# Optimization experiments

Measured on AMD Instinct MI355X. Metric: run time of the kernel, lower is better.

## Reference

```python
import jax, jax.numpy as jnp
import numpy as np
import math

TAU = 1.0          # args.gumbel_tau, used as GMM variance scale in assign()
RD = 64            # args.reduce_dimension
NE = 8             # args.dynamic_nexperts
COMMIT = 0.1       # args.commitment_scale
T, B, C, O = 2048, 8, 512, 512


def setup_inputs() -> dict:
    key = jax.random.key(0)
    ks = jax.random.split(key, 9)
    a = math.sqrt(6.0) / (C + O)  # init for pw_w per dynamic_init_method==1
    return {
        "x": jax.random.normal(ks[0], (T, B, C), jnp.float32),
        "key_feat": jax.random.normal(ks[1], (T, B, C), jnp.float32),  # ignored by forward
        "map_w": jax.random.normal(ks[2], (RD, C), jnp.float32) * math.sqrt(2.0 / (C + RD)),
        "map_b": jnp.zeros((RD,), jnp.float32),
        "centroids": jax.random.normal(ks[3], (NE, RD), jnp.float32) * 0.02,
        "prior": jnp.ones((1, NE), jnp.float32) / NE,
        "pw_w": jax.random.uniform(ks[4], (NE, O * C), jnp.float32, -a, a),
        "bias_w": jax.random.normal(ks[5], (O, C), jnp.float32) * 0.02,
        "bias_b": jnp.zeros((O,), jnp.float32),
    }


def reference(x, key_feat, map_w, map_b, centroids, prior, pw_w, bias_w, bias_b):
    # x: [T, B, C] time-major. key_feat is ignored, matching the original forward.
    Tq, Bq, Cq = x.shape
    N = Tq * Bq
    xf = x.reshape(N, Cq)
    # GMM key projection: [N, RD]
    k = xf @ map_w.T + map_b
    # squared euclid distance to centroids: [N, NE]
    d2 = (jnp.sum(k * k, axis=1, keepdims=True)
          + jnp.sum(centroids * centroids, axis=1)[None, :]
          - 2.0 * (k @ centroids.T))
    # soft GMM responsibilities (training path, no gumbel sampling)
    logresp = (-0.5 * TAU * d2
               - (RD / 2.0) * math.log(2.0 * math.pi * TAU)
               + jnp.log(prior))                                  # [N, NE]
    denom = jax.scipy.special.logsumexp(logresp, axis=-1, keepdims=True)
    resp = jnp.exp(logresp - denom)                               # [N, NE]
    loss = COMMIT * (-jnp.sum(denom))
    # Expert mixture. Original: w = (resp @ pw_w).reshape(T,B,O,C); y = w @ x.
    # Same math, fused order: apply each expert to x, then mix with resp.
    W = pw_w.reshape(NE, O, Cq)
    z = jnp.einsum('ni,eoi->neo', xf, W)        # [N, NE, O] per-expert outputs
    y = jnp.einsum('ne,neo->no', resp, z)       # [N, O]
    y = y.reshape(Tq, Bq, O)
    # dynamic bias: Linear(key_dim -> O) applied to x0
    y = y + x @ bias_w.T + bias_b
    return y, loss
```

## Files before the change

### kernel.cpp

```cpp
#include <hip/hip_runtime.h>
#include <hip/hip_bf16.h>

#define NROWS 16384
#define CC 512
#define OO 512
#define RDIM 64
#define NE 8
#define NEXP 9
#define COMMIT_SCALE 0.1f
#define LOG2PI_TERM 58.81206612509905f

typedef __attribute__((ext_vector_type(8))) short short8;
typedef __attribute__((ext_vector_type(4))) float f32x4;

__device__ __forceinline__ unsigned short f2bf(float f) {
  unsigned int u = __float_as_uint(f);
  u += 0x7fffu + ((u >> 16) & 1u);
  return (unsigned short)(u >> 16);
}
__device__ __forceinline__ unsigned int pkt(float a, float b) {
  return (__float_as_uint(b) & 0xffff0000u) | (__float_as_uint(a) >> 16);
}

__device__ __forceinline__ void gl_lds16(const unsigned short* g, unsigned short* l) {
  __builtin_amdgcn_global_load_lds(
      (const __attribute__((address_space(1))) void*)g,
      (__attribute__((address_space(3))) void*)l, 16, 0, 0);
}

#define P4 524288u
#define B4 65536u
#define NCV ((P4 + B4) / 256u)
#define TB 128u

__global__ __launch_bounds__(256) void k_prep(
    const float* __restrict__ pw, const float* __restrict__ bw,
    const float* __restrict__ mw,
    unsigned short* __restrict__ wb, float* __restrict__ wT4)
{
  unsigned int b = blockIdx.x;
  if (b >= NCV) {
    unsigned int i = (b - NCV) * 256 + threadIdx.x;
    unsigned int j = i >> 9, c = i & 511u;
    wT4[((c >> 2) << 8) + (j << 2) + (c & 3u)] = mw[i];
    return;
  }
  unsigned int i = b * 256 + threadIdx.x;
  const float* src = (i < P4) ? (pw + (size_t)i * 4)
                              : (bw + (size_t)(i - P4) * 4);
  unsigned short* dst = wb + (size_t)i * 4;
  float4 v = *(const float4*)src;
  ushort4 o;
  o.x = f2bf(v.x); o.y = f2bf(v.y); o.z = f2bf(v.z); o.w = f2bf(v.w);
  *(ushort4*)dst = o;
}

__global__ __launch_bounds__(256) void k_assign(
    const float* __restrict__ x,
    const float* __restrict__ wT4,
    const float* __restrict__ map_b,
    const float* __restrict__ cent,
    const float* __restrict__ prior,
    float* __restrict__ resp_out,
    float* __restrict__ loss_acc)
{
  __shared__ float lsum[4];
  const int tid  = threadIdx.x;
  const int wid  = tid >> 6;
  const int lane = tid & 63;
  const int row0 = blockIdx.x * 16 + wid * 4;

  const float* xr0 = x + (size_t)row0 * CC;
  float acc[4] = {0.f, 0.f, 0.f, 0.f};
  #pragma unroll 4
  for (int c0 = 0; c0 < CC; c0 += 4) {
    float4 wv = *(const float4*)&wT4[(c0 << 6) + (lane << 2)];
    #pragma unroll
    for (int r = 0; r < 4; ++r) {
      float4 xv = *(const float4*)(xr0 + r * CC + c0);
      acc[r] += xv.x * wv.x + xv.y * wv.y + xv.z * wv.z + xv.w * wv.w;
    }
  }
  const float mb = map_b[lane];
  float kk[4] = {acc[0] + mb, acc[1] + mb, acc[2] + mb, acc[3] + mb};

  float ce[8], c2[8], lp[8];
  #pragma unroll
  for (int e = 0; e < 8; ++e) {
    ce[e] = cent[e * RDIM + lane];
    float v = ce[e] * ce[e];
    #pragma unroll
    for (int off = 32; off; off >>= 1) v += __shfl_xor(v, off, 64);
    c2[e] = v;
    lp[e] = __logf(prior[e]);
  }

  float dsum = 0.f;
  #pragma unroll
  for (int r = 0; r < 4; ++r) {
    float k = kk[r];
    float v[9];
    v[0] = k * k;
    #pragma unroll
    for (int e = 0; e < 8; ++e) v[e + 1] = k * ce[e];
    #pragma unroll
    for (int off = 32; off; off >>= 1) {
      #pragma unroll
      for (int q = 0; q < 9; ++q) v[q] += __shfl_xor(v[q], off, 64);
    }
    float lr[8], mx = -3.4e38f;
    #pragma unroll
    for (int e = 0; e < 8; ++e) {
      float d2 = v[0] + c2[e] - 2.f * v[e + 1];
      lr[e] = -0.5f * d2 - LOG2PI_TERM + lp[e];
      mx = fmaxf(mx, lr[e]);
    }
    float s = 0.f;
    #pragma unroll
    for (int e = 0; e < 8; ++e) s += __expf(lr[e] - mx);
    float denom = mx + __logf(s);
    dsum += denom;
    float myv = 0.f;
    #pragma unroll
    for (int e = 0; e < 8; ++e) {
      float re = __expf(lr[e] - denom);
      myv = (lane == e) ? re : myv;
    }
    if (lane < 8) resp_out[(size_t)(row0 + r) * NE + lane] = myv;
  }
  if (lane == 0) lsum[wid] = dsum;
  __syncthreads();
  if (tid == 0) {
    float t = lsum[0] + lsum[1] + lsum[2] + lsum[3];
    atomicAdd(loss_acc, -COMMIT_SCALE * t);
  }
}

__global__ __launch_bounds__(256, 2) void k_moe(
    const float* __restrict__ x,
    const unsigned short* __restrict__ wb,
    const float* __restrict__ bb,
    const float* __restrict__ resp,
    const float* __restrict__ loss_acc,
    float* __restrict__ out)
{
  __shared__ unsigned short aT[2][128 * 40];
  __shared__ unsigned short bT[2][128 * 32];
  __shared__ float sc[NEXP * 128];

  const int tid = threadIdx.x;
  const int m0 = blockIdx.x * 128;
  const int o0 = blockIdx.y * 128;

  for (int idx = tid; idx < 128 * NE; idx += 256) {
    int r = idx >> 3, e = idx & 7;
    sc[e * 128 + r] = resp[(size_t)(m0 + r) * NE + e];
  }
  if (tid < 128) sc[8 * 128 + tid] = 1.0f;

  const int lane = tid & 63;
  const int wid = tid >> 6;
  const int wm = (wid & 1) * 64;
  const int wn = (wid >> 1) * 64;
  const int fr = lane & 15;
  const int fq = lane >> 4;

  const int srow = tid >> 1;
  const int scol = (tid & 1) * 16;
  const float4* xb4 = (const float4*)(x + (size_t)(m0 + srow) * CC) + (tid & 1) * 4;

  const int srB = lane >> 2;
  const int gch = (lane & 3) ^ (srB & 3) ^ ((srB >> 2) & 3);
  const size_t b_go = (size_t)(o0 + wid * 32 + srB) * CC + gch * 8;
  const unsigned short* wbp = wb + b_go;
  const size_t row16 = (size_t)16 * CC;
  const int ldsB = wid * 1024;
  const int rchB = (fq ^ (fr & 3) ^ ((fr >> 2) & 3)) * 8;

  f32x4 zero4 = {0.f, 0.f, 0.f, 0.f};
  f32x4 acc[4][4];
  #pragma unroll
  for (int i = 0; i < 4; ++i)
    #pragma unroll
    for (int j = 0; j < 4; ++j) acc[i][j] = zero4;

  __syncthreads();

  float4 cx0 = xb4[0], cx1 = xb4[1], cx2 = xb4[2], cx3 = xb4[3];
  float4 pX0 = xb4[8], pX1 = xb4[9], pX2 = xb4[10], pX3 = xb4[11];

  {
    const float s = sc[srow];
    uint4 w0, w1;
    w0.x = pkt(cx0.x * s, cx0.y * s); w0.y = pkt(cx0.z * s, cx0.w * s);
    w0.z = pkt(cx1.x * s, cx1.y * s); w0.w = pkt(cx1.z * s, cx1.w * s);
    w1.x = pkt(cx2.x * s, cx2.y * s); w1.y = pkt(cx2.z * s, cx2.w * s);
    w1.z = pkt(cx3.x * s, cx3.y * s); w1.w = pkt(cx3.z * s, cx3.w * s);
    *(uint4*)&aT[0][srow * 40 + scol]     = w0;
    *(uint4*)&aT[0][srow * 40 + scol + 8] = w1;
  }
  gl_lds16(wbp,         &bT[0][ldsB]);
  gl_lds16(wbp + row16, &bT[0][ldsB + 512]);

  int cur = 0;
  for (int kk = 0; kk < 16; ++kk) {
    for (int e = 0; e < NEXP; ++e) {
      const int nxt = cur ^ 1;
      __syncthreads();

      if (e < 8) {
        const unsigned short* bn = wbp + ((size_t)(e + 1) << 18) + kk * 32;
        gl_lds16(bn,         &bT[nxt][ldsB]);
        gl_lds16(bn + row16, &bT[nxt][ldsB + 512]);
        const float s = sc[(e + 1) * 128 + srow];
        uint4 w0, w1;
        w0.x = pkt(cx0.x * s, cx0.y * s); w0.y = pkt(cx0.z * s, cx0.w * s);
        w0.z = pkt(cx1.x * s, cx1.y * s); w0.w = pkt(cx1.z * s, cx1.w * s);
        w1.x = pkt(cx2.x * s, cx2.y * s); w1.y = pkt(cx2.z * s, cx2.w * s);
        w1.z = pkt(cx3.x * s, cx3.y * s); w1.w = pkt(cx3.z * s, cx3.w * s);
        *(uint4*)&aT[nxt][srow * 40 + scol]     = w0;
        *(uint4*)&aT[nxt][srow * 40 + scol + 8] = w1;
      } else if (kk < 15) {
        const unsigned short* bn = wbp + (kk + 1) * 32;
        gl_lds16(bn,         &bT[nxt][ldsB]);
        gl_lds16(bn + row16, &bT[nxt][ldsB + 512]);
        const float s = sc[srow];
        uint4 w0, w1;
        w0.x = pkt(pX0.x * s, pX0.y * s); w0.y = pkt(pX0.z * s, pX0.w * s);
        w0.z = pkt(pX1.x * s, pX1.y * s); w0.w = pkt(pX1.z * s, pX1.w * s);
        w1.x = pkt(pX2.x * s, pX2.y * s); w1.y = pkt(pX2.z * s, pX2.w * s);
        w1.z = pkt(pX3.x * s, pX3.y * s); w1.w = pkt(pX3.z * s, pX3.w * s);
        *(uint4*)&aT[nxt][srow * 40 + scol]     = w0;
        *(uint4*)&aT[nxt][srow * 40 + scol + 8] = w1;
        cx0 = pX0; cx1 = pX1; cx2 = pX2; cx3 = pX3;
        if (kk < 14) {
          const int nk = (kk + 2) * 8;
          pX0 = xb4[nk];     pX1 = xb4[nk + 1];
          pX2 = xb4[nk + 2]; pX3 = xb4[nk + 3];
        }
      }

      short8 af[4], bfr[4];
      #pragma unroll
      for (int i = 0; i < 4; ++i)
        af[i] = *(const short8*)&aT[cur][(wm + i * 16 + fr) * 40 + fq * 8];
      #pragma unroll
      for (int j = 0; j < 4; ++j)
        bfr[j] = *(const short8*)&bT[cur][(wn + j * 16 + fr) * 32 + rchB];

      #pragma unroll
      for (int i = 0; i < 4; ++i)
        #pragma unroll
        for (int j = 0; j < 4; ++j)
          acc[i][j] = __builtin_amdgcn_mfma_f32_16x16x32_bf16(af[i], bfr[j], acc[i][j], 0, 0, 0);

      cur = nxt;
    }
  }

  #pragma unroll
  for (int j = 0; j < 4; ++j) {
    const int o = o0 + wn + j * 16 + fr;
    const float bias = bb[o];
    #pragma unroll
    for (int i = 0; i < 4; ++i) {
      #pragma unroll
      for (int r = 0; r < 4; ++r) {
        int m = m0 + wm + i * 16 + fq * 4 + r;
        out[(size_t)m * OO + o] = acc[i][j][r] + bias;
      }
    }
  }

  if (blockIdx.x == 0 && blockIdx.y == 0 && tid == 0)
    out[(size_t)NROWS * OO] = loss_acc[0];
}

extern "C" void kernel_launch(void* const* d_in, const int* in_sizes, int n_in,
                              void* d_out, int out_size, void* d_ws, size_t ws_size,
                              hipStream_t stream) {
  const float* x     = (const float*)d_in[0];
  const float* map_w = (const float*)d_in[2];
  const float* map_b = (const float*)d_in[3];
  const float* cent  = (const float*)d_in[4];
  const float* prior = (const float*)d_in[5];
  const float* pw    = (const float*)d_in[6];
  const float* bw    = (const float*)d_in[7];
  const float* bb    = (const float*)d_in[8];
  float* out = (float*)d_out;

  char* wsp = (char*)d_ws;
  float* resp = (float*)wsp;
  float* loss = (float*)(wsp + 524288);
  unsigned short* wb = (unsigned short*)(wsp + 524304);
  float* wT4 = (float*)(wsp + 524304 + 4718592);

  hipMemsetAsync(loss, 0, sizeof(float), stream);
  k_prep<<<dim3(NCV + TB), dim3(256), 0, stream>>>(pw, bw, map_w, wb, wT4);
  k_assign<<<dim3(NROWS / 16), dim3(256), 0, stream>>>(x, wT4, map_b, cent, prior, resp, loss);
  dim3 grid(NROWS / 128, OO / 128);
  k_moe<<<grid, dim3(256), 0, stream>>>(x, wb, bb, resp, loss, out);
}
```

Measured before the change: 314.8 us.

## Apply responsibilities to per-expert MFMA outputs instead of pre-scaling x tiles

```diff
diff --git a/kernel.cpp b/kernel.cpp
--- a/kernel.cpp
+++ b/kernel.cpp
@@ -144,130 +144,148 @@
     const float* __restrict__ loss_acc,
     float* __restrict__ out)
 {
-  __shared__ unsigned short aT[2][128 * 40];
-  __shared__ unsigned short bT[2][128 * 32];
-  __shared__ float sc[NEXP * 128];
+  __shared__ __align__(16) unsigned short aT[128 * 64];
+  __shared__ __align__(16) unsigned short bT[2][128 * 64];
+  __shared__ float sc[NE * 128];
 
   const int tid = threadIdx.x;
   const int m0 = blockIdx.x * 128;
   const int o0 = blockIdx.y * 128;
+  const int lane = tid & 63;
+  const int wid = tid >> 6;
+  const int fr = lane & 15;
+  const int fq = lane >> 4;
 
   for (int idx = tid; idx < 128 * NE; idx += 256) {
     int r = idx >> 3, e = idx & 7;
     sc[e * 128 + r] = resp[(size_t)(m0 + r) * NE + e];
   }
-  if (tid < 128) sc[8 * 128 + tid] = 1.0f;
-
-  const int lane = tid & 63;
-  const int wid = tid >> 6;
-  const int wm = (wid & 1) * 64;
-  const int wn = (wid >> 1) * 64;
-  const int fr = lane & 15;
-  const int fq = lane >> 4;
-
-  const int srow = tid >> 1;
-  const int scol = (tid & 1) * 16;
-  const float4* xb4 = (const float4*)(x + (size_t)(m0 + srow) * CC) + (tid & 1) * 4;
-
-  const int srB = lane >> 2;
-  const int gch = (lane & 3) ^ (srB & 3) ^ ((srB >> 2) & 3);
-  const size_t b_go = (size_t)(o0 + wid * 32 + srB) * CC + gch * 8;
-  const unsigned short* wbp = wb + b_go;
-  const size_t row16 = (size_t)16 * CC;
-  const int ldsB = wid * 1024;
-  const int rchB = (fq ^ (fr & 3) ^ ((fr >> 2) & 3)) * 8;
-
-  f32x4 zero4 = {0.f, 0.f, 0.f, 0.f};
-  f32x4 acc[4][4];
+
+  const int rl = lane >> 3;
+  const int ch = lane & 7;
+  const unsigned short* wb_t =
+      wb + (size_t)(o0 + wid * 32 + rl) * CC + (ch ^ rl) * 8;
+
+  const int ar = tid >> 1;
+  const int ah = tid & 1;
+  const float* xa = x + (size_t)(m0 + ar) * CC + ah * 32;
+
+  const int s7 = fr & 7;
+  const int ac0 = (fq ^ s7) * 8;
+
+  const f32x4 zero4 = {0.f, 0.f, 0.f, 0.f};
+  f32x4 ySum[8][2];
   #pragma unroll
-  for (int i = 0; i < 4; ++i)
-    #pragma unroll
-    for (int j = 0; j < 4; ++j) acc[i][j] = zero4;
-
-  __syncthreads();
-
-  float4 cx0 = xb4[0], cx1 = xb4[1], cx2 = xb4[2], cx3 = xb4[3];
-  float4 pX0 = xb4[8], pX1 = xb4[9], pX2 = xb4[10], pX3 = xb4[11];
+  for (int i = 0; i < 8; ++i) {
+    ySum[i][0] = zero4; ySum[i][1] = zero4;
+  }
 
   {
-    const float s = sc[srow];
-    uint4 w0, w1;
-    w0.x = pkt(cx0.x * s, cx0.y * s); w0.y = pkt(cx0.z * s, cx0.w * s);
-    w0.z = pkt(cx1.x * s, cx1.y * s); w0.w = pkt(cx1.z * s, cx1.w * s);
-    w1.x = pkt(cx2.x * s, cx2.y * s); w1.y = pkt(cx2.z * s, cx2.w * s);
-    w1.z = pkt(cx3.x * s, cx3.y * s); w1.w = pkt(cx3.z * s, cx3.w * s);
-    *(uint4*)&aT[0][srow * 40 + scol]     = w0;
-    *(uint4*)&aT[0][srow * 40 + scol + 8] = w1;
-  }
-  gl_lds16(wbp,         &bT[0][ldsB]);
-  gl_lds16(wbp + row16, &bT[0][ldsB + 512]);
-
+    const float4* xp = (const float4*)xa;
+    #pragma unroll
+    for (int q = 0; q < 4; ++q) {
+      float4 f0 = xp[2 * q], f1 = xp[2 * q + 1];
+      uint4 w;
+      w.x = pkt(f0.x, f0.y); w.y = pkt(f0.z, f0.w);
+      w.z = pkt(f1.x, f1.y); w.w = pkt(f1.z, f1.w);
+      *(uint4*)&aT[ar * 64 + (((ah * 4 + q) ^ (ar & 7)) << 3)] = w;
+    }
+    #pragma unroll
+    for (int q = 0; q < 4; ++q)
+      gl_lds16(wb_t + q * 4096, &bT[0][wid * 2048 + q * 512]);
+  }
+
+  short8 af[16];
+  float4 xf[8];
   int cur = 0;
-  for (int kk = 0; kk < 16; ++kk) {
+
+  #pragma unroll 1
+  for (int kk = 0; kk < 8; ++kk) {
+    #pragma unroll 1
     for (int e = 0; e < NEXP; ++e) {
-      const int nxt = cur ^ 1;
       __syncthreads();
 
+      if (e < 8 || kk < 7) {
+        const int ne = (e < 8) ? e + 1 : 0;
+        const int nk = (e < 8) ? kk : kk + 1;
+        const unsigned short* bn = wb_t + ((size_t)ne << 18) + nk * 64;
+        #pragma unroll
+        for (int q = 0; q < 4; ++q)
+          gl_lds16(bn + q * 4096, &bT[cur ^ 1][wid * 2048 + q * 512]);
+      }
+
+      if (e == 0) {
+        #pragma unroll
+        for (int i = 0; i < 8; ++i) {
+          const int rb = (i * 16 + fr) * 64;
+          af[2 * i]     = *(const short8*)&aT[rb + ac0];
+          af[2 * i + 1] = *(const short8*)&aT[rb + (ac0 ^ 32)];
+        }
+        if (kk < 7) {
+          const float4* xp = (const float4*)(xa + (kk + 1) * 64);
+          #pragma unroll
+          for (int q = 0; q < 8; ++q) xf[q] = xp[q];
+        }
+      } else if (e == 1 && kk < 7) {
+        #pragma unroll
+        for (int q = 0; q < 4; ++q) {
+          uint4 w;
+          w.x = pkt(xf[2 * q].x,     xf[2 * q].y);
+          w.y = pkt(xf[2 * q].z,     xf[2 * q].w);
+          w.z = pkt(xf[2 * q + 1].x, xf[2 * q + 1].y);
+          w.w = pkt(xf[2 * q + 1].z, xf[2 * q + 1].w);
+          *(uint4*)&aT[ar * 64 + (((ah * 4 + q) ^ (ar & 7)) << 3)] = w;
+        }
+      }
+
+      short8 bfv[4];
+      const unsigned short* bc = &bT[cur][0];
+      #pragma unroll
+      for (int j = 0; j < 2; ++j) {
+        const int rb = (wid * 32 + j * 16 + fr) * 64;
+        bfv[2 * j]     = *(const short8*)&bc[rb + ac0];
+        bfv[2 * j + 1] = *(const short8*)&bc[rb + (ac0 ^ 32)];
+      }
+
       if (e < 8) {
-        const unsigned short* bn = wbp + ((size_t)(e + 1) << 18) + kk * 32;
-        gl_lds16(bn,         &bT[nxt][ldsB]);
-        gl_lds16(bn + row16, &bT[nxt][ldsB + 512]);
-        const float s = sc[(e + 1) * 128 + srow];
-        uint4 w0, w1;
-        w0.x = pkt(cx0.x * s, cx0.y * s); w0.y = pkt(cx0.z * s, cx0.w * s);
-        w0.z = pkt(cx1.x * s, cx1.y * s); w0.w = pkt(cx1.z * s, cx1.w * s);
-        w1.x = pkt(cx2.x * s, cx2.y * s); w1.y = pkt(cx2.z * s, cx2.w * s);
-        w1.z = pkt(cx3.x * s, cx3.y * s); w1.w = pkt(cx3.z * s, cx3.w * s);
-        *(uint4*)&aT[nxt][srow * 40 + scol]     = w0;
-        *(uint4*)&aT[nxt][srow * 40 + scol + 8] = w1;
-      } else if (kk < 15) {
-        const unsigned short* bn = wbp + (kk + 1) * 32;
-        gl_lds16(bn,         &bT[nxt][ldsB]);
-        gl_lds16(bn + row16, &bT[nxt][ldsB + 512]);
-        const float s = sc[srow];
-        uint4 w0, w1;
-        w0.x = pkt(pX0.x * s, pX0.y * s); w0.y = pkt(pX0.z * s, pX0.w * s);
-        w0.z = pkt(pX1.x * s, pX1.y * s); w0.w = pkt(pX1.z * s, pX1.w * s);
-        w1.x = pkt(pX2.x * s, pX2.y * s); w1.y = pkt(pX2.z * s, pX2.w * s);
-        w1.z = pkt(pX3.x * s, pX3.y * s); w1.w = pkt(pX3.z * s, pX3.w * s);
-        *(uint4*)&aT[nxt][srow * 40 + scol]     = w0;
-        *(uint4*)&aT[nxt][srow * 40 + scol + 8] = w1;
-        cx0 = pX0; cx1 = pX1; cx2 = pX2; cx3 = pX3;
-        if (kk < 14) {
-          const int nk = (kk + 2) * 8;
-          pX0 = xb4[nk];     pX1 = xb4[nk + 1];
-          pX2 = xb4[nk + 2]; pX3 = xb4[nk + 3];
-        }
-      }
-
-      short8 af[4], bfr[4];
-      #pragma unroll
-      for (int i = 0; i < 4; ++i)
-        af[i] = *(const short8*)&aT[cur][(wm + i * 16 + fr) * 40 + fq * 8];
-      #pragma unroll
-      for (int j = 0; j < 4; ++j)
-        bfr[j] = *(const short8*)&bT[cur][(wn + j * 16 + fr) * 32 + rchB];
-
-      #pragma unroll
-      for (int i = 0; i < 4; ++i)
-        #pragma unroll
-        for (int j = 0; j < 4; ++j)
-          acc[i][j] = __builtin_amdgcn_mfma_f32_16x16x32_bf16(af[i], bfr[j], acc[i][j], 0, 0, 0);
-
-      cur = nxt;
+        #pragma unroll
+        for (int i = 0; i < 8; ++i) {
+          const f32x4 s = *(const f32x4*)&sc[e * 128 + i * 16 + fq * 4];
+          #pragma unroll
+          for (int j = 0; j < 2; ++j) {
+            f32x4 t = __builtin_amdgcn_mfma_f32_16x16x32_bf16(
+                af[2 * i], bfv[2 * j], zero4, 0, 0, 0);
+            t = __builtin_amdgcn_mfma_f32_16x16x32_bf16(
+                af[2 * i + 1], bfv[2 * j + 1], t, 0, 0, 0);
+            ySum[i][j] += s * t;
+          }
+        }
+      } else {
+        #pragma unroll
+        for (int i = 0; i < 8; ++i) {
+          #pragma unroll
+          for (int j = 0; j < 2; ++j) {
+            ySum[i][j] = __builtin_amdgcn_mfma_f32_16x16x32_bf16(
+                af[2 * i], bfv[2 * j], ySum[i][j], 0, 0, 0);
+            ySum[i][j] = __builtin_amdgcn_mfma_f32_16x16x32_bf16(
+                af[2 * i + 1], bfv[2 * j + 1], ySum[i][j], 0, 0, 0);
+          }
+        }
+      }
+      cur ^= 1;
     }
   }
 
   #pragma unroll
-  for (int j = 0; j < 4; ++j) {
-    const int o = o0 + wn + j * 16 + fr;
+  for (int j = 0; j < 2; ++j) {
+    const int o = o0 + wid * 32 + j * 16 + fr;
     const float bias = bb[o];
     #pragma unroll
-    for (int i = 0; i < 4; ++i) {
+    for (int i = 0; i < 8; ++i) {
       #pragma unroll
       for (int r = 0; r < 4; ++r) {
-        int m = m0 + wm + i * 16 + fq * 4 + r;
-        out[(size_t)m * OO + o] = acc[i][j][r] + bias;
+        int m = m0 + i * 16 + fq * 4 + r;
+        out[(size_t)m * OO + o] = ySum[i][j][r] + bias;
       }
     }
   }
```

After: 311.1 us. Within noise of the previous version (-1.2%).

## Drop LDS staging in MoE GEMM; load MFMA fragments directly from global

Applied to the files above, without the earlier changes.

```diff
diff --git a/kernel.cpp b/kernel.cpp
--- a/kernel.cpp
+++ b/kernel.cpp
@@ -20,12 +20,6 @@
 }
 __device__ __forceinline__ unsigned int pkt(float a, float b) {
   return (__float_as_uint(b) & 0xffff0000u) | (__float_as_uint(a) >> 16);
-}
-
-__device__ __forceinline__ void gl_lds16(const unsigned short* g, unsigned short* l) {
-  __builtin_amdgcn_global_load_lds(
-      (const __attribute__((address_space(1))) void*)g,
-      (__attribute__((address_space(3))) void*)l, 16, 0, 0);
 }
 
 #define P4 524288u
@@ -136,6 +130,87 @@
   }
 }
 
+#define MFm(A,B,C) __builtin_amdgcn_mfma_f32_16x16x32_bf16((A),(B),(C),0,0,0)
+
+#define BLOAD(D, EOFF) do {                                         \
+    D##0 = *(const short8*)(bkb + (EOFF));                          \
+    D##1 = *(const short8*)(bkb + (EOFF) + 8192);                   \
+    D##2 = *(const short8*)(bkb + (EOFF) + 16384);                  \
+    D##3 = *(const short8*)(bkb + (EOFF) + 24576);                  \
+  } while (0)
+
+#define AROW(II, EE, B_) do {                                       \
+    const float s_ = sv[II][EE];                                    \
+    uint4 w_;                                                       \
+    w_.x = pkt(xc[II][0].x * s_, xc[II][0].y * s_);                 \
+    w_.y = pkt(xc[II][0].z * s_, xc[II][0].w * s_);                 \
+    w_.z = pkt(xc[II][1].x * s_, xc[II][1].y * s_);                 \
+    w_.w = pkt(xc[II][1].z * s_, xc[II][1].w * s_);                 \
+    const short8 a_ = *(const short8*)&w_;                          \
+    acc[II][0] = MFm(a_, B_##0, acc[II][0]);                        \
+    acc[II][1] = MFm(a_, B_##1, acc[II][1]);                        \
+    acc[II][2] = MFm(a_, B_##2, acc[II][2]);                        \
+    acc[II][3] = MFm(a_, B_##3, acc[II][3]);                        \
+  } while (0)
+
+#define PH(EE, B_) do {                                             \
+    AROW(0, EE, B_); AROW(1, EE, B_);                               \
+    AROW(2, EE, B_); AROW(3, EE, B_);                               \
+  } while (0)
+
+#define ARAWV(II) do {                                              \
+    uint4 w_;                                                       \
+    w_.x = pkt(xc[II][0].x, xc[II][0].y);                           \
+    w_.y = pkt(xc[II][0].z, xc[II][0].w);                           \
+    w_.z = pkt(xc[II][1].x, xc[II][1].y);                           \
+    w_.w = pkt(xc[II][1].z, xc[II][1].w);                           \
+    ar##II = *(const short8*)&w_;                                   \
+  } while (0)
+
+#define XNEXT(II) do {                                              \
+    xc[II][0] = *(const float4*)(xp##II + 32);                      \
+    xc[II][1] = *(const float4*)(xp##II + 36);                      \
+    xp##II += 32;                                                   \
+  } while (0)
+
+#define PH8(BC, BN, LAST) do {                                      \
+    short8 ar0, ar1, ar2, ar3;                                      \
+    ARAWV(0); ARAWV(1); ARAWV(2); ARAWV(3);                         \
+    if (!(LAST)) {                                                  \
+      XNEXT(0); XNEXT(1); XNEXT(2); XNEXT(3);                       \
+      BLOAD(BN, 32);                                                \
+      bkb += 32;                                                    \
+    }                                                               \
+    acc[0][0] = MFm(ar0, BC##0, acc[0][0]);                         \
+    acc[0][1] = MFm(ar0, BC##1, acc[0][1]);                         \
+    acc[0][2] = MFm(ar0, BC##2, acc[0][2]);                         \
+    acc[0][3] = MFm(ar0, BC##3, acc[0][3]);                         \
+    acc[1][0] = MFm(ar1, BC##0, acc[1][0]);                         \
+    acc[1][1] = MFm(ar1, BC##1, acc[1][1]);                         \
+    acc[1][2] = MFm(ar1, BC##2, acc[1][2]);                         \
+    acc[1][3] = MFm(ar1, BC##3, acc[1][3]);                         \
+    acc[2][0] = MFm(ar2, BC##0, acc[2][0]);                         \
+    acc[2][1] = MFm(ar2, BC##1, acc[2][1]);                         \
+    acc[2][2] = MFm(ar2, BC##2, acc[2][2]);                         \
+    acc[2][3] = MFm(ar2, BC##3, acc[2][3]);                         \
+    acc[3][0] = MFm(ar3, BC##0, acc[3][0]);                         \
+    acc[3][1] = MFm(ar3, BC##1, acc[3][1]);                         \
+    acc[3][2] = MFm(ar3, BC##2, acc[3][2]);                         \
+    acc[3][3] = MFm(ar3, BC##3, acc[3][3]);                         \
+  } while (0)
+
+#define KKBODY(PA_, PB_, LAST) do {                                 \
+    BLOAD(PB_, 262144);       PH(0, PA_);                           \
+    BLOAD(PA_, 2 * 262144);   PH(1, PB_);                           \
+    BLOAD(PB_, 3 * 262144);   PH(2, PA_);                           \
+    BLOAD(PA_, 4 * 262144);   PH(3, PB_);                           \
+    BLOAD(PB_, 5 * 262144);   PH(4, PA_);                           \
+    BLOAD(PA_, 6 * 262144);   PH(5, PB_);                           \
+    BLOAD(PB_, 7 * 262144);   PH(6, PA_);                           \
+    BLOAD(PA_, 8 * 262144);   PH(7, PB_);                           \
+    PH8(PA_, PB_, LAST);                                            \
+  } while (0)
+
 __global__ __launch_bounds__(256, 2) void k_moe(
     const float* __restrict__ x,
     const unsigned short* __restrict__ wb,
@@ -144,20 +219,9 @@
     const float* __restrict__ loss_acc,
     float* __restrict__ out)
 {
-  __shared__ unsigned short aT[2][128 * 40];
-  __shared__ unsigned short bT[2][128 * 32];
-  __shared__ float sc[NEXP * 128];
-
   const int tid = threadIdx.x;
   const int m0 = blockIdx.x * 128;
   const int o0 = blockIdx.y * 128;
-
-  for (int idx = tid; idx < 128 * NE; idx += 256) {
-    int r = idx >> 3, e = idx & 7;
-    sc[e * 128 + r] = resp[(size_t)(m0 + r) * NE + e];
-  }
-  if (tid < 128) sc[8 * 128 + tid] = 1.0f;
-
   const int lane = tid & 63;
   const int wid = tid >> 6;
   const int wm = (wid & 1) * 64;
@@ -165,97 +229,50 @@
   const int fr = lane & 15;
   const int fq = lane >> 4;
 
-  const int srow = tid >> 1;
-  const int scol = (tid & 1) * 16;
-  const float4* xb4 = (const float4*)(x + (size_t)(m0 + srow) * CC) + (tid & 1) * 4;
-
-  const int srB = lane >> 2;
-  const int gch = (lane & 3) ^ (srB & 3) ^ ((srB >> 2) & 3);
-  const size_t b_go = (size_t)(o0 + wid * 32 + srB) * CC + gch * 8;
-  const unsigned short* wbp = wb + b_go;
-  const size_t row16 = (size_t)16 * CC;
-  const int ldsB = wid * 1024;
-  const int rchB = (fq ^ (fr & 3) ^ ((fr >> 2) & 3)) * 8;
-
-  f32x4 zero4 = {0.f, 0.f, 0.f, 0.f};
+  const unsigned short* bkb = wb + (size_t)(o0 + wn + fr) * CC + fq * 8;
+
+  const float* xp0 = x + (size_t)(m0 + wm +  0 + fr) * CC + fq * 8;
+  const float* xp1 = x + (size_t)(m0 + wm + 16 + fr) * CC + fq * 8;
+  const float* xp2 = x + (size_t)(m0 + wm + 32 + fr) * CC + fq * 8;
+  const float* xp3 = x + (size_t)(m0 + wm + 48 + fr) * CC + fq * 8;
+
+  float sv[4][8];
+  {
+    const float* rp = resp + (size_t)(m0 + wm + fr) * NE;
+    #define SVLOAD(II)                                              \
+      { float4 lo_ = *(const float4*)(rp + (II) * 128);             \
+        float4 hi_ = *(const float4*)(rp + (II) * 128 + 4);         \
+        sv[II][0] = lo_.x; sv[II][1] = lo_.y;                       \
+        sv[II][2] = lo_.z; sv[II][3] = lo_.w;                       \
+        sv[II][4] = hi_.x; sv[II][5] = hi_.y;                       \
+        sv[II][6] = hi_.z; sv[II][7] = hi_.w; }
+    SVLOAD(0) SVLOAD(1) SVLOAD(2) SVLOAD(3)
+    #undef SVLOAD
+  }
+
+  float4 xc[4][2];
+  xc[0][0] = *(const float4*)xp0; xc[0][1] = *(const float4*)(xp0 + 4);
+  xc[1][0] = *(const float4*)xp1; xc[1][1] = *(const float4*)(xp1 + 4);
+  xc[2][0] = *(const float4*)xp2; xc[2][1] = *(const float4*)(xp2 + 4);
+  xc[3][0] = *(const float4*)xp3; xc[3][1] = *(const float4*)(xp3 + 4);
+
   f32x4 acc[4][4];
   #pragma unroll
   for (int i = 0; i < 4; ++i)
     #pragma unroll
-    for (int j = 0; j < 4; ++j) acc[i][j] = zero4;
-
-  __syncthreads();
-
-  float4 cx0 = xb4[0], cx1 = xb4[1], cx2 = xb4[2], cx3 = xb4[3];
-  float4 pX0 = xb4[8], pX1 = xb4[9], pX2 = xb4[10], pX3 = xb4[11];
-
-  {
-    const float s = sc[srow];
-    uint4 w0, w1;
-    w0.x = pkt(cx0.x * s, cx0.y * s); w0.y = pkt(cx0.z * s, cx0.w * s);
-    w0.z = pkt(cx1.x * s, cx1.y * s); w0.w = pkt(cx1.z * s, cx1.w * s);
-    w1.x = pkt(cx2.x * s, cx2.y * s); w1.y = pkt(cx2.z * s, cx2.w * s);
-    w1.z = pkt(cx3.x * s, cx3.y * s); w1.w = pkt(cx3.z * s, cx3.w * s);
-    *(uint4*)&aT[0][srow * 40 + scol]     = w0;
-    *(uint4*)&aT[0][srow * 40 + scol + 8] = w1;
-  }
-  gl_lds16(wbp,         &bT[0][ldsB]);
-  gl_lds16(wbp + row16, &bT[0][ldsB + 512]);
-
-  int cur = 0;
-  for (int kk = 0; kk < 16; ++kk) {
-    for (int e = 0; e < NEXP; ++e) {
-      const int nxt = cur ^ 1;
-      __syncthreads();
-
-      if (e < 8) {
-        const unsigned short* bn = wbp + ((size_t)(e + 1) << 18) + kk * 32;
-        gl_lds16(bn,         &bT[nxt][ldsB]);
-        gl_lds16(bn + row16, &bT[nxt][ldsB + 512]);
-        const float s = sc[(e + 1) * 128 + srow];
-        uint4 w0, w1;
-        w0.x = pkt(cx0.x * s, cx0.y * s); w0.y = pkt(cx0.z * s, cx0.w * s);
-        w0.z = pkt(cx1.x * s, cx1.y * s); w0.w = pkt(cx1.z * s, cx1.w * s);
-        w1.x = pkt(cx2.x * s, cx2.y * s); w1.y = pkt(cx2.z * s, cx2.w * s);
-        w1.z = pkt(cx3.x * s, cx3.y * s); w1.w = pkt(cx3.z * s, cx3.w * s);
-        *(uint4*)&aT[nxt][srow * 40 + scol]     = w0;
-        *(uint4*)&aT[nxt][srow * 40 + scol + 8] = w1;
-      } else if (kk < 15) {
-        const unsigned short* bn = wbp + (kk + 1) * 32;
-        gl_lds16(bn,         &bT[nxt][ldsB]);
-        gl_lds16(bn + row16, &bT[nxt][ldsB + 512]);
-        const float s = sc[srow];
-        uint4 w0, w1;
-        w0.x = pkt(pX0.x * s, pX0.y * s); w0.y = pkt(pX0.z * s, pX0.w * s);
-        w0.z = pkt(pX1.x * s, pX1.y * s); w0.w = pkt(pX1.z * s, pX1.w * s);
-        w1.x = pkt(pX2.x * s, pX2.y * s); w1.y = pkt(pX2.z * s, pX2.w * s);
-        w1.z = pkt(pX3.x * s, pX3.y * s); w1.w = pkt(pX3.z * s, pX3.w * s);
-        *(uint4*)&aT[nxt][srow * 40 + scol]     = w0;
-        *(uint4*)&aT[nxt][srow * 40 + scol + 8] = w1;
-        cx0 = pX0; cx1 = pX1; cx2 = pX2; cx3 = pX3;
-        if (kk < 14) {
-          const int nk = (kk + 2) * 8;
-          pX0 = xb4[nk];     pX1 = xb4[nk + 1];
-          pX2 = xb4[nk + 2]; pX3 = xb4[nk + 3];
-        }
-      }
-
-      short8 af[4], bfr[4];
-      #pragma unroll
-      for (int i = 0; i < 4; ++i)
-        af[i] = *(const short8*)&aT[cur][(wm + i * 16 + fr) * 40 + fq * 8];
-      #pragma unroll
-      for (int j = 0; j < 4; ++j)
-        bfr[j] = *(const short8*)&bT[cur][(wn + j * 16 + fr) * 32 + rchB];
-
-      #pragma unroll
-      for (int i = 0; i < 4; ++i)
-        #pragma unroll
-        for (int j = 0; j < 4; ++j)
-          acc[i][j] = __builtin_amdgcn_mfma_f32_16x16x32_bf16(af[i], bfr[j], acc[i][j], 0, 0, 0);
-
-      cur = nxt;
-    }
+    for (int j = 0; j < 4; ++j) {
+      f32x4 z = {0.f, 0.f, 0.f, 0.f};
+      acc[i][j] = z;
+    }
+
+  short8 pA0, pA1, pA2, pA3;
+  short8 pB0, pB1, pB2, pB3;
+  BLOAD(pA, 0);
+
+  #pragma unroll 1
+  for (int kk2 = 0; kk2 < 8; ++kk2) {
+    KKBODY(pA, pB, 0);
+    KKBODY(pB, pA, (kk2 == 7));
   }
 
   #pragma unroll
```

Result: slower. 440.3 us (+39.8%).
